# Kernel tuning notes

Hardware: AMD Instinct MI355X
Metric: run time of the kernel (lower is better)

Reference implementation:

```python
import jax, jax.numpy as jnp
import numpy as np

B, C = 20000, 8          # trees, children (leaves) per tree
WORD, TAG, MEM = 300, 50, 150


def gru_cell(x, h, w_ih, w_hh, b_ih, b_hh):
    # torch.nn.GRUCell math; gate order r, z, n
    gi = x @ w_ih.T + b_ih
    gh = h @ w_hh.T + b_hh
    ir, iz, i_n = jnp.split(gi, 3, axis=-1)
    hr, hz, hn = jnp.split(gh, 3, axis=-1)
    r = jax.nn.sigmoid(ir + hr)
    z = jax.nn.sigmoid(iz + hz)
    n = jnp.tanh(i_n + r * hn)
    return (1.0 - z) * n + z * h


def setup_inputs() -> dict:
    key = jax.random.key(0)
    ks = jax.random.split(key, 16)
    s = 0.05  # small init scale for weights
    return {
        "embs": jax.random.normal(ks[0], (B, C, WORD), jnp.float32),
        "tags": jax.random.normal(ks[1], (B, C, TAG), jnp.float32),
        "tag_parent": jax.random.normal(ks[2], (B, TAG), jnp.float32),
        "w_ih_leaf": jax.random.normal(ks[3], (3 * MEM, WORD + TAG), jnp.float32) * s,
        "w_hh_leaf": jax.random.normal(ks[4], (3 * MEM, MEM), jnp.float32) * s,
        "b_ih_leaf": jax.random.normal(ks[5], (3 * MEM,), jnp.float32) * s,
        "b_hh_leaf": jax.random.normal(ks[6], (3 * MEM,), jnp.float32) * s,
        "w_ih_child": jax.random.normal(ks[7], (3 * MEM, MEM + 2 * TAG), jnp.float32) * s,
        "w_hh_child": jax.random.normal(ks[8], (3 * MEM, MEM), jnp.float32) * s,
        "b_ih_child": jax.random.normal(ks[9], (3 * MEM,), jnp.float32) * s,
        "b_hh_child": jax.random.normal(ks[10], (3 * MEM,), jnp.float32) * s,
        "w_ih_node": jax.random.normal(ks[11], (3 * MEM, 1), jnp.float32) * s,
        "w_hh_node": jax.random.normal(ks[12], (3 * MEM, MEM), jnp.float32) * s,
        "b_ih_node": jax.random.normal(ks[13], (3 * MEM,), jnp.float32) * s,
        "b_hh_node": jax.random.normal(ks[14], (3 * MEM,), jnp.float32) * s,
    }


def reference(embs, tags, tag_parent,
              w_ih_leaf, w_hh_leaf, b_ih_leaf, b_hh_leaf,
              w_ih_child, w_hh_child, b_ih_child, b_hh_child,
              w_ih_node, w_hh_node, b_ih_node, b_hh_node):
    # 1) all leaves at once: GRUCell(concat(word, tag), h=0)  -> [B, C, MEM]
    x_leaf = jnp.concatenate([embs, tags], axis=-1)            # [B, C, WORD+TAG]
    h0 = jnp.zeros((B, C, MEM), x_leaf.dtype)
    leaf_h = gru_cell(x_leaf, h0, w_ih_leaf, w_hh_leaf, b_ih_leaf, b_hh_leaf)

    # 2) child inputs: concat(child state, child tag, parent tag)  -> [B, C, MEM+2*TAG]
    tp = jnp.broadcast_to(tag_parent[:, None, :], (B, C, TAG))
    x_child = jnp.concatenate([leaf_h, tags, tp], axis=-1)

    # 3) sequential left-to-right fold over children with children GRUCell
    def step(h, x_i):
        h_new = gru_cell(x_i, h, w_ih_child, w_hh_child, b_ih_child, b_hh_child)
        return h_new, None

    h_init = jnp.zeros((B, MEM), x_leaf.dtype)
    h_final, _ = jax.lax.scan(step, h_init, jnp.swapaxes(x_child, 0, 1))  # scan over C

    # 4) node GRUCell with x = zeros(1)
    x_zeros = jnp.zeros((B, 1), x_leaf.dtype)
    root = gru_cell(x_zeros, h_final, w_ih_node, w_hh_node, b_ih_node, b_hh_node)
    return root  # [B, MEM]
```

## Files before the change

### kernel.cpp

```cpp
#include <hip/hip_runtime.h>


typedef _Float16 f16;
typedef _Float16 f16x4 __attribute__((ext_vector_type(4)));
typedef _Float16 f16x8 __attribute__((ext_vector_type(8)));
typedef float f32x4 __attribute__((ext_vector_type(4)));

namespace {

constexpr int NTREE = 20000;
constexpr int CCH   = 8;
constexpr int WORD  = 300;
constexpr int TAGD  = 50;
constexpr int MEMD  = 150;
constexpr int NBLK  = 250;
constexpr int LBLK  = 313;

constexpr int KT_L = 11;
constexpr int KT_I = 8;
constexpr int KT_H = 5;
constexpr int KT_N = 5;
constexpr int NTILE = 30;

constexpr size_t OFF_WL   = 0;
constexpr size_t OFF_WI   = OFF_WL + (size_t)KT_L * NTILE * 64 * 16;
constexpr size_t OFF_WH   = OFF_WI + (size_t)KT_I * NTILE * 64 * 16;
constexpr size_t OFF_WN   = OFF_WH + (size_t)KT_H * NTILE * 64 * 16;
constexpr size_t OFF_BIAS = OFF_WN + (size_t)KT_N * NTILE * 64 * 16;
constexpr size_t OFF_DATA = OFF_BIAS + 16 * 160 * 4;

constexpr size_t TG_BYTES = 15360;
constexpr size_t C_STRIDE = (size_t)1250 * TG_BYTES;
constexpr size_t GI_BYTES = (size_t)CCH * C_STRIDE;
constexpr size_t WS_R3    = OFF_DATA + GI_BYTES;
constexpr int    HW_S  = 152;
constexpr size_t WS_R2 = OFF_DATA + (size_t)CCH * NTREE * HW_S * 2;


__device__ __forceinline__ float sigmoid_f(float x) {
  return 1.0f / (1.0f + __expf(-x));
}
__device__ __forceinline__ float tanh_f(float x) {
  float ax = fabsf(x);
  float e  = __expf(-2.0f * ax);
  float t  = (1.0f - e) / (1.0f + e);
  return copysignf(t, x);
}

__global__ void prep_kernel(const float* __restrict__ w_ih_leaf,
                            const float* __restrict__ b_ih_leaf,
                            const float* __restrict__ b_hh_leaf,
                            const float* __restrict__ w_ih_child,
                            const float* __restrict__ w_hh_child,
                            const float* __restrict__ b_ih_child,
                            const float* __restrict__ b_hh_child,
                            const float* __restrict__ w_hh_node,
                            const float* __restrict__ b_ih_node,
                            const float* __restrict__ b_hh_node,
                            char* __restrict__ ws) {
  const int NWL = KT_L * NTILE * 64;
  const int NWI = KT_I * NTILE * 64;
  const int NWH = KT_H * NTILE * 64;
  const int NWN = KT_N * NTILE * 64;
  int t = blockIdx.x * blockDim.x + threadIdx.x;

  if (t < NWL) {
    int kt = t / (NTILE * 64), rem = t % (NTILE * 64);
    int nt = rem / 64, l = rem % 64;
    int gate = nt / 10, jt = nt % 10;
    int j = jt * 16 + (l & 15);
    bool valid = j < MEMD;
    int g = gate * MEMD + (valid ? j : 0);
    f16x8 v;
#pragma unroll
    for (int e = 0; e < 8; ++e) {
      int k = kt * 32 + ((l >> 4) * 8) + e;
      v[e] = (f16)((valid && k < WORD + TAGD) ? w_ih_leaf[g * (WORD + TAGD) + k] : 0.0f);
    }
    ((f16x8*)(ws + OFF_WL))[t] = v;
    return;
  }
  t -= NWL;
  if (t < NWI) {
    int kt = t / (NTILE * 64), rem = t % (NTILE * 64);
    int nt = rem / 64, l = rem % 64;
    int gate = nt / 10, jt = nt % 10;
    int j = jt * 16 + (l & 15);
    bool valid = j < MEMD;
    int g = gate * MEMD + (valid ? j : 0);
    f16x8 v;
#pragma unroll
    for (int e = 0; e < 8; ++e) {
      int k = kt * 32 + ((l >> 4) * 8) + e;
      int src = (k < 150) ? k : (k >= 152 && k < 252) ? (k - 2) : -1;
      v[e] = (f16)((valid && src >= 0) ? w_ih_child[g * 250 + src] : 0.0f);
    }
    ((f16x8*)(ws + OFF_WI))[t] = v;
    return;
  }
  t -= NWI;
  if (t < NWH) {
    int kt = t / (NTILE * 64), rem = t % (NTILE * 64);
    int nt = rem / 64, l = rem % 64;
    int gate = nt / 10, jt = nt % 10;
    int j = jt * 16 + (l & 15);
    bool valid = j < MEMD;
    int g = gate * MEMD + (valid ? j : 0);
    f16x8 v;
#pragma unroll
    for (int e = 0; e < 8; ++e) {
      int k = kt * 32 + ((l >> 4) * 8) + e;
      v[e] = (f16)((valid && k < MEMD) ? w_hh_child[g * MEMD + k] : 0.0f);
    }
    ((f16x8*)(ws + OFF_WH))[t] = v;
    return;
  }
  t -= NWH;
  if (t < NWN) {
    int kt = t / (NTILE * 64), rem = t % (NTILE * 64);
    int nt = rem / 64, l = rem % 64;
    int gate = nt / 10, jt = nt % 10;
    int j = jt * 16 + (l & 15);
    bool valid = j < MEMD;
    int g = gate * MEMD + (valid ? j : 0);
    f16x8 v;
#pragma unroll
    for (int e = 0; e < 8; ++e) {
      int k = kt * 32 + ((l >> 4) * 8) + e;
      v[e] = (f16)((valid && k < MEMD) ? w_hh_node[g * MEMD + k] : 0.0f);
    }
    ((f16x8*)(ws + OFF_WN))[t] = v;
    return;
  }
  t -= NWN;
  if (t < 16 * 160) {
    int arr = t / 160, j = t % 160;
    float v = 0.0f;
    if (j < MEMD) {
      switch (arr) {
        case 0:  v = b_ih_leaf[j] + b_hh_leaf[j]; break;
        case 1:  v = b_ih_leaf[MEMD + j] + b_hh_leaf[MEMD + j]; break;
        case 2:  v = b_ih_leaf[2 * MEMD + j]; break;
        case 3:  v = b_hh_leaf[2 * MEMD + j]; break;
        case 4:  v = b_ih_child[j] + b_hh_child[j]; break;
        case 5:  v = b_ih_child[MEMD + j] + b_hh_child[MEMD + j]; break;
        case 6:  v = b_ih_child[2 * MEMD + j]; break;
        case 7:  v = b_hh_child[2 * MEMD + j]; break;
        case 8:  v = b_ih_node[j] + b_hh_node[j]; break;
        case 9:  v = b_ih_node[MEMD + j] + b_hh_node[MEMD + j]; break;
        case 10: v = b_ih_node[2 * MEMD + j]; break;
        case 11: v = b_hh_node[2 * MEMD + j]; break;
        case 12: v = b_ih_child[j]; break;
        case 13: v = b_ih_child[MEMD + j]; break;
        case 14: v = b_hh_child[j]; break;
        case 15: v = b_hh_child[MEMD + j]; break;
      }
    }
    ((float*)(ws + OFF_BIAS))[arr * 160 + j] = v;
  }
}

__global__ __launch_bounds__(640)
void leaf6_kernel(const float* __restrict__ embs,
                  const float* __restrict__ tags,
                  const float* __restrict__ tag_parent,
                  char* __restrict__ ws) {
  __shared__ f16 buf[64 * 360];
  f16* xle = buf;
  f16* xch = buf;

  const f16x8* WL   = (const f16x8*)(ws + OFF_WL);
  const f16x8* WI   = (const f16x8*)(ws + OFF_WI);
  const float* BIAS = (const float*)(ws + OFF_BIAS);

  const int tid = threadIdx.x, lane = tid & 63, w = tid >> 6;
  const int blk = blockIdx.x, c = blockIdx.y, t0 = blk * 64;
  const int arow = lane & 15, acol8 = (lane >> 4) * 8, qrow = (lane >> 4) * 4;
  const int j = w * 16 + arow;
  const bool jok = j < MEMD;

  for (int i = tid; i < 64 * 75; i += 640) {
    int r = i / 75, k4 = i - r * 75;
    int row = min(t0 + r, NTREE - 1);
    float4 v = *(const float4*)(embs + ((size_t)row * CCH + c) * WORD + 4 * k4);
    f16* p = xle + r * 360 + 4 * k4;
    p[0] = (f16)v.x; p[1] = (f16)v.y; p[2] = (f16)v.z; p[3] = (f16)v.w;
  }
  for (int i = tid; i < 64 * 25; i += 640) {
    int r = i / 25, k2 = i - r * 25;
    int row = min(t0 + r, NTREE - 1);
    float2 v = *(const float2*)(tags + ((size_t)row * CCH + c) * TAGD + 2 * k2);
    xle[r * 360 + 300 + 2 * k2]     = (f16)v.x;
    xle[r * 360 + 300 + 2 * k2 + 1] = (f16)v.y;
  }
  if (tid < 64) {
    xle[tid * 360 + 350] = (f16)0.0f;
    xle[tid * 360 + 351] = (f16)0.0f;
  }
  __syncthreads();

  f32x4 acc[3][4];
#pragma unroll
  for (int g = 0; g < 3; ++g)
#pragma unroll
    for (int m = 0; m < 4; ++m) acc[g][m] = 0.f;

  for (int kt = 0; kt < KT_L; ++kt) {
    f16x8 a0 = *(const f16x8*)(xle + kt * 32 + acol8 + (arow)      * 360);
    f16x8 a1 = *(const f16x8*)(xle + kt * 32 + acol8 + (16 + arow) * 360);
    f16x8 a2 = *(const f16x8*)(xle + kt * 32 + acol8 + (32 + arow) * 360);
    f16x8 a3 = *(const f16x8*)(xle + kt * 32 + acol8 + (48 + arow) * 360);
#pragma unroll
    for (int g = 0; g < 3; ++g) {
      f16x8 b = WL[(kt * NTILE + g * 10 + w) * 64 + lane];
      acc[g][0] = __builtin_amdgcn_mfma_f32_16x16x32_f16(a0, b, acc[g][0], 0, 0, 0);
      acc[g][1] = __builtin_amdgcn_mfma_f32_16x16x32_f16(a1, b, acc[g][1], 0, 0, 0);
      acc[g][2] = __builtin_amdgcn_mfma_f32_16x16x32_f16(a2, b, acc[g][2], 0, 0, 0);
      acc[g][3] = __builtin_amdgcn_mfma_f32_16x16x32_f16(a3, b, acc[g][3], 0, 0, 0);
    }
  }
  __syncthreads();

  {
    const float bLr = BIAS[j], bLz = BIAS[160 + j];
    const float bLi = BIAS[320 + j], bLh = BIAS[480 + j];
#pragma unroll
    for (int m = 0; m < 4; ++m)
#pragma unroll
      for (int q = 0; q < 4; ++q) {
        int row = 16 * m + qrow + q;
        float rg = sigmoid_f(acc[0][m][q] + bLr);
        float zg = sigmoid_f(acc[1][m][q] + bLz);
        float ng = tanh_f(acc[2][m][q] + bLi + rg * bLh);
        if (jok) xch[row * 264 + j] = (f16)((1.0f - zg) * ng);
      }
  }
  for (int i = tid; i < 64 * 25; i += 640) {
    int r = i / 25, k2 = i - r * 25;
    int row = min(t0 + r, NTREE - 1);
    float2 v = *(const float2*)(tags + ((size_t)row * CCH + c) * TAGD + 2 * k2);
    xch[r * 264 + 152 + 2 * k2] = (f16)v.x;
    xch[r * 264 + 153 + 2 * k2] = (f16)v.y;
  }
  for (int i = tid; i < 64 * 25; i += 640) {
    int r = i / 25, k2 = i - r * 25;
    int row = min(t0 + r, NTREE - 1);
    float2 v = *(const float2*)(tag_parent + (size_t)row * TAGD + 2 * k2);
    xch[r * 264 + 202 + 2 * k2] = (f16)v.x;
    xch[r * 264 + 203 + 2 * k2] = (f16)v.y;
  }
  for (int i = tid; i < 64 * 6; i += 640) {
    int r = i / 6, k = i - r * 6;
    int col = (k < 2) ? (150 + k) : (250 + k);
    xch[r * 264 + col] = (f16)0.0f;
  }
  __syncthreads();

#pragma unroll
  for (int g = 0; g < 3; ++g)
#pragma unroll
    for (int m = 0; m < 4; ++m) acc[g][m] = 0.f;

  for (int kt = 0; kt < KT_I; ++kt) {
    f16x8 a0 = *(const f16x8*)(xch + kt * 32 + acol8 + (arow)      * 264);
    f16x8 a1 = *(const f16x8*)(xch + kt * 32 + acol8 + (16 + arow) * 264);
    f16x8 a2 = *(const f16x8*)(xch + kt * 32 + acol8 + (32 + arow) * 264);
    f16x8 a3 = *(const f16x8*)(xch + kt * 32 + acol8 + (48 + arow) * 264);
#pragma unroll
    for (int g = 0; g < 3; ++g) {
      f16x8 b = WI[(kt * NTILE + g * 10 + w) * 64 + lane];
      acc[g][0] = __builtin_amdgcn_mfma_f32_16x16x32_f16(a0, b, acc[g][0], 0, 0, 0);
      acc[g][1] = __builtin_amdgcn_mfma_f32_16x16x32_f16(a1, b, acc[g][1], 0, 0, 0);
      acc[g][2] = __builtin_amdgcn_mfma_f32_16x16x32_f16(a2, b, acc[g][2], 0, 0, 0);
      acc[g][3] = __builtin_amdgcn_mfma_f32_16x16x32_f16(a3, b, acc[g][3], 0, 0, 0);
    }
  }

  {
    const float bi[3] = {BIAS[12 * 160 + j], BIAS[13 * 160 + j], BIAS[6 * 160 + j]};
#pragma unroll
    for (int m = 0; m < 4; ++m) {
      if (t0 + 16 * m < NTREE) {
        int tg = blk * 4 + m;
        char* base = ws + OFF_DATA + (size_t)c * C_STRIDE + (size_t)tg * TG_BYTES +
                     (size_t)lane * 8;
#pragma unroll
        for (int g = 0; g < 3; ++g) {
          f16x4 v;
#pragma unroll
          for (int q = 0; q < 4; ++q) v[q] = (f16)(acc[g][m][q] + bi[g]);
          *(f16x4*)(base + (size_t)(g * 10 + w) * 512) = v;
        }
      }
    }
  }
}

__global__ __launch_bounds__(640, 1)
void fold6_kernel(const char* __restrict__ ws,
                  float* __restrict__ out) {
  __shared__ f16 hls[80 * 168];

  const f16x8* WH   = (const f16x8*)(ws + OFF_WH);
  const f16x8* WN   = (const f16x8*)(ws + OFF_WN);
  const float* BIAS = (const float*)(ws + OFF_BIAS);

  const int tid = threadIdx.x, lane = tid & 63, w = tid >> 6;
  const int blk = blockIdx.x, t0 = blk * 80;
  const int arow = lane & 15, acol8 = (lane >> 4) * 8, qrow = (lane >> 4) * 4;
  const int j = w * 16 + arow;
  const bool jok = j < MEMD;

  const float bhr = BIAS[14 * 160 + j], bhz = BIAS[15 * 160 + j], bhn = BIAS[7 * 160 + j];
  const float bNr = BIAS[8 * 160 + j],  bNz = BIAS[9 * 160 + j];
  const float bNi = BIAS[10 * 160 + j], bNh = BIAS[11 * 160 + j];

  for (int i = tid; i < 80 * 18; i += 640) {
    int r = i / 18;
    hls[r * 168 + 150 + (i - r * 18)] = (f16)0.0f;
  }

  f16x8 whr[5], whz[5], whn[5];
#pragma unroll
  for (int kt = 0; kt < KT_H; ++kt) {
    whr[kt] = WH[(kt * NTILE + w) * 64 + lane];
    whz[kt] = WH[(kt * NTILE + 10 + w) * 64 + lane];
    whn[kt] = WH[(kt * NTILE + 20 + w) * 64 + lane];
  }

  const char* gbase = ws + OFF_DATA + (size_t)(blk * 5) * TG_BYTES +
                      (size_t)w * 512 + (size_t)lane * 8;

  f32x4 hp[5];
#pragma unroll
  for (int m = 0; m < 5; ++m) hp[m] = 0.f;

#pragma unroll
  for (int c = 0; c < CCH; ++c) {
    f16x4 gbuf[15];
#pragma unroll
    for (int m = 0; m < 5; ++m)
#pragma unroll
      for (int g = 0; g < 3; ++g)
        gbuf[m * 3 + g] = *(const f16x4*)(gbase + (size_t)c * C_STRIDE +
                                          (size_t)m * TG_BYTES + (size_t)g * 5120);

    f32x4 aR[5], aZ[5], aNh[5];
#pragma unroll
    for (int m = 0; m < 5; ++m) { aR[m] = 0.f; aZ[m] = 0.f; aNh[m] = 0.f; }

    if (c != 0) {
#pragma unroll
      for (int kt = 0; kt < KT_H; ++kt) {
        const f16* ab = hls + kt * 32 + acol8;
#pragma unroll
        for (int m = 0; m < 5; ++m) {
          f16x8 a = *(const f16x8*)(ab + (16 * m + arow) * 168);
          aR[m]  = __builtin_amdgcn_mfma_f32_16x16x32_f16(a, whr[kt], aR[m], 0, 0, 0);
          aZ[m]  = __builtin_amdgcn_mfma_f32_16x16x32_f16(a, whz[kt], aZ[m], 0, 0, 0);
          aNh[m] = __builtin_amdgcn_mfma_f32_16x16x32_f16(a, whn[kt], aNh[m], 0, 0, 0);
        }
      }
      __syncthreads();
    }

#pragma unroll
    for (int m = 0; m < 5; ++m)
#pragma unroll
      for (int q = 0; q < 4; ++q) {
        int row = 16 * m + qrow + q;
        float rg = sigmoid_f((float)gbuf[m * 3 + 0][q] + aR[m][q] + bhr);
        float zg = sigmoid_f((float)gbuf[m * 3 + 1][q] + aZ[m][q] + bhz);
        float ng = tanh_f((float)gbuf[m * 3 + 2][q] + rg * (aNh[m][q] + bhn));
        float h  = (1.0f - zg) * ng + zg * hp[m][q];
        hp[m][q] = h;
        if (jok) hls[row * 168 + j] = (f16)h;
      }
    __syncthreads();
  }

  f32x4 aR[5], aZ[5], aNh[5];
#pragma unroll
  for (int m = 0; m < 5; ++m) { aR[m] = 0.f; aZ[m] = 0.f; aNh[m] = 0.f; }
  for (int kt = 0; kt < KT_N; ++kt) {
    f16x8 br = WN[(kt * NTILE + w) * 64 + lane];
    f16x8 bz = WN[(kt * NTILE + 10 + w) * 64 + lane];
    f16x8 bn = WN[(kt * NTILE + 20 + w) * 64 + lane];
    const f16* ab = hls + kt * 32 + acol8;
#pragma unroll
    for (int m = 0; m < 5; ++m) {
      f16x8 a = *(const f16x8*)(ab + (16 * m + arow) * 168);
      aR[m]  = __builtin_amdgcn_mfma_f32_16x16x32_f16(a, br, aR[m], 0, 0, 0);
      aZ[m]  = __builtin_amdgcn_mfma_f32_16x16x32_f16(a, bz, aZ[m], 0, 0, 0);
      aNh[m] = __builtin_amdgcn_mfma_f32_16x16x32_f16(a, bn, aNh[m], 0, 0, 0);
    }
  }
#pragma unroll
  for (int m = 0; m < 5; ++m)
#pragma unroll
    for (int q = 0; q < 4; ++q) {
      int row = 16 * m + qrow + q;
      float rg = sigmoid_f(aR[m][q] + bNr);
      float zg = sigmoid_f(aZ[m][q] + bNz);
      float ng = tanh_f(bNi + rg * (aNh[m][q] + bNh));
      float o  = (1.0f - zg) * ng + zg * hp[m][q];
      if (jok) out[(size_t)(t0 + row) * MEMD + j] = o;
    }
}

namespace r2 {

__global__ __launch_bounds__(640)
void leaf_kernel(const float* __restrict__ embs,
                 const float* __restrict__ tags,
                 char* __restrict__ ws) {
  __shared__ f16 xle[80 * 360];
  const f16x8* WL   = (const f16x8*)(ws + OFF_WL);
  const float* BIAS = (const float*)(ws + OFF_BIAS);
  f16* hws = (f16*)(ws + OFF_DATA);

  const int tid = threadIdx.x, lane = tid & 63, w = tid >> 6;
  const int c = blockIdx.y, t0 = blockIdx.x * 80;
  const int arow = lane & 15, acol8 = (lane >> 4) * 8, qrow = (lane >> 4) * 4;
  const int j = w * 16 + (lane & 15);

  for (int i = tid; i < 80 * 150; i += 640) {
    int r = i / 150, k2 = i - r * 150;
    float2 v = *(const float2*)(embs + ((size_t)(t0 + r) * CCH + c) * WORD + 2 * k2);
    xle[r * 360 + 2 * k2]     = (f16)v.x;
    xle[r * 360 + 2 * k2 + 1] = (f16)v.y;
  }
  for (int i = tid; i < 80 * 25; i += 640) {
    int r = i / 25, k2 = i - r * 25;
    float2 v = *(const float2*)(tags + ((size_t)(t0 + r) * CCH + c) * TAGD + 2 * k2);
    xle[r * 360 + 300 + 2 * k2]     = (f16)v.x;
    xle[r * 360 + 300 + 2 * k2 + 1] = (f16)v.y;
  }
  for (int i = tid; i < 80; i += 640) {
    xle[i * 360 + 350] = (f16)0.0f;
    xle[i * 360 + 351] = (f16)0.0f;
  }
  __syncthreads();

  f32x4 aR[5], aZ[5], aN[5];
#pragma unroll
  for (int m = 0; m < 5; ++m) { aR[m] = 0.f; aZ[m] = 0.f; aN[m] = 0.f; }
  for (int kt = 0; kt < KT_L; ++kt) {
    f16x8 br = WL[(kt * NTILE + w) * 64 + lane];
    f16x8 bz = WL[(kt * NTILE + 10 + w) * 64 + lane];
    f16x8 bn = WL[(kt * NTILE + 20 + w) * 64 + lane];
    const f16* ab = xle + kt * 32 + acol8;
#pragma unroll
    for (int m = 0; m < 5; ++m) {
      f16x8 a = *(const f16x8*)(ab + (16 * m + arow) * 360);
      aR[m] = __builtin_amdgcn_mfma_f32_16x16x32_f16(a, br, aR[m], 0, 0, 0);
      aZ[m] = __builtin_amdgcn_mfma_f32_16x16x32_f16(a, bz, aZ[m], 0, 0, 0);
      aN[m] = __builtin_amdgcn_mfma_f32_16x16x32_f16(a, bn, aN[m], 0, 0, 0);
    }
  }
  const float bLr = BIAS[j], bLz = BIAS[160 + j], bLi = BIAS[320 + j], bLh = BIAS[480 + j];
#pragma unroll
  for (int m = 0; m < 5; ++m) {
#pragma unroll
    for (int q = 0; q < 4; ++q) {
      int row = 16 * m + qrow + q;
      float rg = sigmoid_f(aR[m][q] + bLr);
      float zg = sigmoid_f(aZ[m][q] + bLz);
      float ng = tanh_f(aN[m][q] + bLi + rg * bLh);
      float h  = (1.0f - zg) * ng;
      if (j < HW_S)
        hws[((size_t)c * NTREE + t0 + row) * HW_S + j] = (f16)(j < MEMD ? h : 0.0f);
    }
  }
}

__global__ __launch_bounds__(640)
void fold_kernel(const float* __restrict__ tags,
                 const float* __restrict__ tag_parent,
                 const char* __restrict__ ws,
                 float* __restrict__ out) {
  extern __shared__ char fsm[];
  f16* xch0 = (f16*)fsm;
  f16* xch1 = xch0 + 80 * 264;
  f16* hls  = xch1 + 80 * 264;

  const f16x8* WI   = (const f16x8*)(ws + OFF_WI);
  const f16x8* WH   = (const f16x8*)(ws + OFF_WH);
  const f16x8* WN   = (const f16x8*)(ws + OFF_WN);
  const float* BIAS = (const float*)(ws + OFF_BIAS);
  const f16*   hws  = (const f16*)(ws + OFF_DATA);

  const int tid = threadIdx.x, lane = tid & 63, w = tid >> 6;
  const int t0 = blockIdx.x * 80;
  const int arow = lane & 15, acol8 = (lane >> 4) * 8, qrow = (lane >> 4) * 4;
  const int j = w * 16 + (lane & 15);
  const bool jok = j < MEMD;

  const float bCr = BIAS[4 * 160 + j], bCz = BIAS[5 * 160 + j];
  const float bCi = BIAS[6 * 160 + j], bCh = BIAS[7 * 160 + j];
  const float bNr = BIAS[8 * 160 + j], bNz = BIAS[9 * 160 + j];
  const float bNi = BIAS[10 * 160 + j], bNh = BIAS[11 * 160 + j];

  for (int i = tid; i < 1680; i += 640) ((int4*)hls)[i] = make_int4(0, 0, 0, 0);
  for (int i = tid; i < 80 * 25; i += 640) {
    int r = i / 25, k2 = i - r * 25;
    float2 v = *(const float2*)(tag_parent + (size_t)(t0 + r) * TAGD + 2 * k2);
    f16 a = (f16)v.x, b = (f16)v.y;
    xch0[r * 264 + 202 + 2 * k2] = a; xch0[r * 264 + 203 + 2 * k2] = b;
    xch1[r * 264 + 202 + 2 * k2] = a; xch1[r * 264 + 203 + 2 * k2] = b;
  }
  for (int i = tid; i < 80 * 4; i += 640) {
    int r = i >> 2, k = i & 3;
    xch0[r * 264 + 252 + k] = (f16)0.0f;
    xch1[r * 264 + 252 + k] = (f16)0.0f;
  }
#pragma unroll
  for (int s = 0; s < 3; ++s) {
    int i = tid + 640 * s;
    if (i < 1520) {
      int r = i / 19, q = i - r * 19;
      *(f16x8*)(xch0 + r * 264 + 8 * q) =
          *(const f16x8*)(hws + ((size_t)(t0 + r)) * HW_S + 8 * q);
    }
  }
#pragma unroll
  for (int s = 0; s < 4; ++s) {
    int i = tid + 640 * s;
    if (i < 2000) {
      int r = i / 25, k2 = i - r * 25;
      float2 v = *(const float2*)(tags + ((size_t)(t0 + r) * CCH) * TAGD + 2 * k2);
      xch0[r * 264 + 152 + 2 * k2] = (f16)v.x;
      xch0[r * 264 + 153 + 2 * k2] = (f16)v.y;
    }
  }
  __syncthreads();

  f32x4 hp[5];
#pragma unroll
  for (int m = 0; m < 5; ++m) hp[m] = 0.f;

  f16* xc = xch0;
  f16* xa = xch1;

  for (int c = 0; c < CCH; ++c) {
    f16x8 ph[3];
    float2 pt[4];
    if (c < 7) {
#pragma unroll
      for (int s = 0; s < 3; ++s) {
        int i = tid + 640 * s;
        if (i < 1520) {
          int r = i / 19, q = i - r * 19;
          ph[s] = *(const f16x8*)(hws + ((size_t)(c + 1) * NTREE + t0 + r) * HW_S + 8 * q);
        }
      }
#pragma unroll
      for (int s = 0; s < 4; ++s) {
        int i = tid + 640 * s;
        if (i < 2000) {
          int r = i / 25, k2 = i - r * 25;
          pt[s] = *(const float2*)(tags + ((size_t)(t0 + r) * CCH + (c + 1)) * TAGD + 2 * k2);
        }
      }
    }

    f32x4 aR[5], aZ[5], aNi[5], aNh[5];
#pragma unroll
    for (int m = 0; m < 5; ++m) { aR[m] = 0.f; aZ[m] = 0.f; aNi[m] = 0.f; aNh[m] = 0.f; }
    for (int kt = 0; kt < KT_I; ++kt) {
      f16x8 br = WI[(kt * NTILE + w) * 64 + lane];
      f16x8 bz = WI[(kt * NTILE + 10 + w) * 64 + lane];
      f16x8 bn = WI[(kt * NTILE + 20 + w) * 64 + lane];
      const f16* ab = xc + kt * 32 + acol8;
#pragma unroll
      for (int m = 0; m < 5; ++m) {
        f16x8 a = *(const f16x8*)(ab + (16 * m + arow) * 264);
        aR[m]  = __builtin_amdgcn_mfma_f32_16x16x32_f16(a, br, aR[m], 0, 0, 0);
        aZ[m]  = __builtin_amdgcn_mfma_f32_16x16x32_f16(a, bz, aZ[m], 0, 0, 0);
        aNi[m] = __builtin_amdgcn_mfma_f32_16x16x32_f16(a, bn, aNi[m], 0, 0, 0);
      }
    }
    for (int kt = 0; kt < KT_H; ++kt) {
      f16x8 br = WH[(kt * NTILE + w) * 64 + lane];
      f16x8 bz = WH[(kt * NTILE + 10 + w) * 64 + lane];
      f16x8 bn = WH[(kt * NTILE + 20 + w) * 64 + lane];
      const f16* ab = hls + kt * 32 + acol8;
#pragma unroll
      for (int m = 0; m < 5; ++m) {
        f16x8 a = *(const f16x8*)(ab + (16 * m + arow) * 168);
        aR[m]  = __builtin_amdgcn_mfma_f32_16x16x32_f16(a, br, aR[m], 0, 0, 0);
        aZ[m]  = __builtin_amdgcn_mfma_f32_16x16x32_f16(a, bz, aZ[m], 0, 0, 0);
        aNh[m] = __builtin_amdgcn_mfma_f32_16x16x32_f16(a, bn, aNh[m], 0, 0, 0);
      }
    }
    __syncthreads();

    if (c < 7) {
#pragma unroll
      for (int s = 0; s < 3; ++s) {
        int i = tid + 640 * s;
        if (i < 1520) {
          int r = i / 19, q = i - r * 19;
          *(f16x8*)(xa + r * 264 + 8 * q) = ph[s];
        }
      }
#pragma unroll
      for (int s = 0; s < 4; ++s) {
        int i = tid + 640 * s;
        if (i < 2000) {
          int r = i / 25, k2 = i - r * 25;
          xa[r * 264 + 152 + 2 * k2] = (f16)pt[s].x;
          xa[r * 264 + 153 + 2 * k2] = (f16)pt[s].y;
        }
      }
    }

#pragma unroll
    for (int m = 0; m < 5; ++m) {
#pragma unroll
      for (int q = 0; q < 4; ++q) {
        int row = 16 * m + qrow + q;
        float rg = sigmoid_f(aR[m][q] + bCr);
        float zg = sigmoid_f(aZ[m][q] + bCz);
        float ng = tanh_f(aNi[m][q] + bCi + rg * (aNh[m][q] + bCh));
        float h  = (1.0f - zg) * ng + zg * hp[m][q];
        hp[m][q] = h;
        if (jok) hls[row * 168 + j] = (f16)h;
      }
    }
    __syncthreads();
    f16* tsw = xc; xc = xa; xa = tsw;
  }

  f32x4 aR[5], aZ[5], aNh[5];
#pragma unroll
  for (int m = 0; m < 5; ++m) { aR[m] = 0.f; aZ[m] = 0.f; aNh[m] = 0.f; }
  for (int kt = 0; kt < KT_N; ++kt) {
    f16x8 br = WN[(kt * NTILE + w) * 64 + lane];
    f16x8 bz = WN[(kt * NTILE + 10 + w) * 64 + lane];
    f16x8 bn = WN[(kt * NTILE + 20 + w) * 64 + lane];
    const f16* ab = hls + kt * 32 + acol8;
#pragma unroll
    for (int m = 0; m < 5; ++m) {
      f16x8 a = *(const f16x8*)(ab + (16 * m + arow) * 168);
      aR[m]  = __builtin_amdgcn_mfma_f32_16x16x32_f16(a, br, aR[m], 0, 0, 0);
      aZ[m]  = __builtin_amdgcn_mfma_f32_16x16x32_f16(a, bz, aZ[m], 0, 0, 0);
      aNh[m] = __builtin_amdgcn_mfma_f32_16x16x32_f16(a, bn, aNh[m], 0, 0, 0);
    }
  }
#pragma unroll
  for (int m = 0; m < 5; ++m) {
#pragma unroll
    for (int q = 0; q < 4; ++q) {
      int row = 16 * m + qrow + q;
      float rg = sigmoid_f(aR[m][q] + bNr);
      float zg = sigmoid_f(aZ[m][q] + bNz);
      float ng = tanh_f(bNi + rg * (aNh[m][q] + bNh));
      float o  = (1.0f - zg) * ng + zg * hp[m][q];
      if (jok) out[(size_t)(t0 + row) * MEMD + j] = o;
    }
  }
}

}

}

extern "C" void kernel_launch(void* const* d_in, const int* in_sizes, int n_in,
                              void* d_out, int out_size, void* d_ws, size_t ws_size,
                              hipStream_t stream) {
  const float* embs       = (const float*)d_in[0];
  const float* tags       = (const float*)d_in[1];
  const float* tag_parent = (const float*)d_in[2];
  const float* w_ih_leaf  = (const float*)d_in[3];
  const float* b_ih_leaf  = (const float*)d_in[5];
  const float* b_hh_leaf  = (const float*)d_in[6];
  const float* w_ih_child = (const float*)d_in[7];
  const float* w_hh_child = (const float*)d_in[8];
  const float* b_ih_child = (const float*)d_in[9];
  const float* b_hh_child = (const float*)d_in[10];
  const float* w_hh_node  = (const float*)d_in[12];
  const float* b_ih_node  = (const float*)d_in[13];
  const float* b_hh_node  = (const float*)d_in[14];
  float* out = (float*)d_out;
  char*  ws  = (char*)d_ws;

  prep_kernel<<<228, 256, 0, stream>>>(w_ih_leaf, b_ih_leaf, b_hh_leaf,
                                       w_ih_child, w_hh_child, b_ih_child, b_hh_child,
                                       w_hh_node, b_ih_node, b_hh_node, ws);

  if (ws_size >= WS_R3) {
    leaf6_kernel<<<dim3(LBLK, CCH), 640, 0, stream>>>(embs, tags, tag_parent, ws);
    fold6_kernel<<<NBLK, 640, 0, stream>>>(ws, out);
  } else {
    r2::leaf_kernel<<<dim3(250, CCH), 640, 0, stream>>>(embs, tags, ws);
    constexpr int FOLD_LDS = (2 * 80 * 264 + 80 * 168) * 2;
    hipFuncSetAttribute((const void*)r2::fold_kernel,
                        hipFuncAttributeMaxDynamicSharedMemorySize, FOLD_LDS);
    r2::fold_kernel<<<250, 640, FOLD_LDS, stream>>>(tags, tag_parent, ws, out);
  }
}
```

Measured before the change: 391.1 us.

## Process two children per leaf block with register prefetch; double-buffer fold hidden state

The leaf kernel now handles two children per block. The second child's embeddings and tags are prefetched into registers while the first child's GEMMs run, and tag_parent is loaded once and reused for both children. The fold kernel ping-pongs the hidden state between two LDS buffers, which removes one barrier per step. In exchange the leaf grid is halved to about 1252 blocks of 640 threads, with more LDS and register pressure per block (launch_bounds 640,1), which may reduce how well latency is hidden.

```diff
diff --git a/kernel.cpp b/kernel.cpp
--- a/kernel.cpp
+++ b/kernel.cpp
@@ -160,56 +160,93 @@
   }
 }
 
-__global__ __launch_bounds__(640)
-void leaf6_kernel(const float* __restrict__ embs,
-                  const float* __restrict__ tags,
-                  const float* __restrict__ tag_parent,
-                  char* __restrict__ ws) {
-  __shared__ f16 buf[64 * 360];
-  f16* xle = buf;
-  f16* xch = buf;
+__global__ __launch_bounds__(640, 1)
+void leaf11_kernel(const float* __restrict__ embs,
+                   const float* __restrict__ tags,
+                   const float* __restrict__ tag_parent,
+                   char* __restrict__ ws) {
+  __shared__ f16 bufA[64 * 360];
+  __shared__ f16 bufB[64 * 360];
 
   const f16x8* WL   = (const f16x8*)(ws + OFF_WL);
   const f16x8* WI   = (const f16x8*)(ws + OFF_WI);
   const float* BIAS = (const float*)(ws + OFF_BIAS);
 
   const int tid = threadIdx.x, lane = tid & 63, w = tid >> 6;
-  const int blk = blockIdx.x, c = blockIdx.y, t0 = blk * 64;
+  const int blk = blockIdx.x, t0 = blk * 64;
+  const int c0 = blockIdx.y * 2, c1 = c0 + 1;
   const int arow = lane & 15, acol8 = (lane >> 4) * 8, qrow = (lane >> 4) * 4;
   const int j = w * 16 + arow;
   const bool jok = j < MEMD;
 
+  const float bLr = BIAS[j], bLz = BIAS[160 + j];
+  const float bLi = BIAS[320 + j], bLh = BIAS[480 + j];
+  const float biC[3] = {BIAS[12 * 160 + j], BIAS[13 * 160 + j], BIAS[6 * 160 + j]};
+
+  float2 tp[3];
+#pragma unroll
+  for (int s = 0; s < 3; ++s) {
+    int i = tid + 640 * s;
+    tp[s] = make_float2(0.0f, 0.0f);
+    if (i < 1600) {
+      int r = i / 25, k2 = i - (i / 25) * 25;
+      int row = min(t0 + r, NTREE - 1);
+      tp[s] = *(const float2*)(tag_parent + (size_t)row * TAGD + 2 * k2);
+    }
+  }
+
   for (int i = tid; i < 64 * 75; i += 640) {
     int r = i / 75, k4 = i - r * 75;
     int row = min(t0 + r, NTREE - 1);
-    float4 v = *(const float4*)(embs + ((size_t)row * CCH + c) * WORD + 4 * k4);
-    f16* p = xle + r * 360 + 4 * k4;
+    float4 v = *(const float4*)(embs + ((size_t)row * CCH + c0) * WORD + 4 * k4);
+    f16* p = bufA + r * 360 + 4 * k4;
     p[0] = (f16)v.x; p[1] = (f16)v.y; p[2] = (f16)v.z; p[3] = (f16)v.w;
   }
   for (int i = tid; i < 64 * 25; i += 640) {
     int r = i / 25, k2 = i - r * 25;
     int row = min(t0 + r, NTREE - 1);
-    float2 v = *(const float2*)(tags + ((size_t)row * CCH + c) * TAGD + 2 * k2);
-    xle[r * 360 + 300 + 2 * k2]     = (f16)v.x;
-    xle[r * 360 + 300 + 2 * k2 + 1] = (f16)v.y;
+    float2 v = *(const float2*)(tags + ((size_t)row * CCH + c0) * TAGD + 2 * k2);
+    bufA[r * 360 + 300 + 2 * k2]     = (f16)v.x;
+    bufA[r * 360 + 300 + 2 * k2 + 1] = (f16)v.y;
   }
   if (tid < 64) {
-    xle[tid * 360 + 350] = (f16)0.0f;
-    xle[tid * 360 + 351] = (f16)0.0f;
+    bufA[tid * 360 + 350] = (f16)0.0f;
+    bufA[tid * 360 + 351] = (f16)0.0f;
   }
   __syncthreads();
 
+  float4 pe[8];
+  float2 pt[3];
+#pragma unroll
+  for (int s = 0; s < 8; ++s) {
+    int i = tid + 640 * s;
+    if (i < 4800) {
+      int r = i / 75, k4 = i - r * 75;
+      int row = min(t0 + r, NTREE - 1);
+      pe[s] = *(const float4*)(embs + ((size_t)row * CCH + c1) * WORD + 4 * k4);
+    }
+  }
+#pragma unroll
+  for (int s = 0; s < 3; ++s) {
+    int i = tid + 640 * s;
+    if (i < 1600) {
+      int r = i / 25, k2 = i - (i / 25) * 25;
+      int row = min(t0 + r, NTREE - 1);
+      pt[s] = *(const float2*)(tags + ((size_t)row * CCH + c1) * TAGD + 2 * k2);
+    }
+  }
+
   f32x4 acc[3][4];
+
 #pragma unroll
   for (int g = 0; g < 3; ++g)
 #pragma unroll
     for (int m = 0; m < 4; ++m) acc[g][m] = 0.f;
-
   for (int kt = 0; kt < KT_L; ++kt) {
-    f16x8 a0 = *(const f16x8*)(xle + kt * 32 + acol8 + (arow)      * 360);
-    f16x8 a1 = *(const f16x8*)(xle + kt * 32 + acol8 + (16 + arow) * 360);
-    f16x8 a2 = *(const f16x8*)(xle + kt * 32 + acol8 + (32 + arow) * 360);
-    f16x8 a3 = *(const f16x8*)(xle + kt * 32 + acol8 + (48 + arow) * 360);
+    f16x8 a0 = *(const f16x8*)(bufA + kt * 32 + acol8 + (arow)      * 360);
+    f16x8 a1 = *(const f16x8*)(bufA + kt * 32 + acol8 + (16 + arow) * 360);
+    f16x8 a2 = *(const f16x8*)(bufA + kt * 32 + acol8 + (32 + arow) * 360);
+    f16x8 a3 = *(const f16x8*)(bufA + kt * 32 + acol8 + (48 + arow) * 360);
 #pragma unroll
     for (int g = 0; g < 3; ++g) {
       f16x8 b = WL[(kt * NTILE + g * 10 + w) * 64 + lane];
@@ -221,38 +258,58 @@
   }
   __syncthreads();
 
-  {
-    const float bLr = BIAS[j], bLz = BIAS[160 + j];
-    const float bLi = BIAS[320 + j], bLh = BIAS[480 + j];
-#pragma unroll
-    for (int m = 0; m < 4; ++m)
-#pragma unroll
-      for (int q = 0; q < 4; ++q) {
-        int row = 16 * m + qrow + q;
-        float rg = sigmoid_f(acc[0][m][q] + bLr);
-        float zg = sigmoid_f(acc[1][m][q] + bLz);
-        float ng = tanh_f(acc[2][m][q] + bLi + rg * bLh);
-        if (jok) xch[row * 264 + j] = (f16)((1.0f - zg) * ng);
-      }
-  }
+#pragma unroll
+  for (int s = 0; s < 8; ++s) {
+    int i = tid + 640 * s;
+    if (i < 4800) {
+      int r = i / 75, k4 = i - (i / 75) * 75;
+      f16* p = bufB + r * 360 + 4 * k4;
+      p[0] = (f16)pe[s].x; p[1] = (f16)pe[s].y; p[2] = (f16)pe[s].z; p[3] = (f16)pe[s].w;
+    }
+  }
+#pragma unroll
+  for (int s = 0; s < 3; ++s) {
+    int i = tid + 640 * s;
+    if (i < 1600) {
+      int r = i / 25, k2 = i - (i / 25) * 25;
+      bufB[r * 360 + 300 + 2 * k2]     = (f16)pt[s].x;
+      bufB[r * 360 + 300 + 2 * k2 + 1] = (f16)pt[s].y;
+    }
+  }
+  if (tid < 64) {
+    bufB[tid * 360 + 350] = (f16)0.0f;
+    bufB[tid * 360 + 351] = (f16)0.0f;
+  }
+#pragma unroll
+  for (int m = 0; m < 4; ++m)
+#pragma unroll
+    for (int q = 0; q < 4; ++q) {
+      int row = 16 * m + qrow + q;
+      float rg = sigmoid_f(acc[0][m][q] + bLr);
+      float zg = sigmoid_f(acc[1][m][q] + bLz);
+      float ng = tanh_f(acc[2][m][q] + bLi + rg * bLh);
+      if (jok) bufA[row * 264 + j] = (f16)((1.0f - zg) * ng);
+    }
   for (int i = tid; i < 64 * 25; i += 640) {
     int r = i / 25, k2 = i - r * 25;
     int row = min(t0 + r, NTREE - 1);
-    float2 v = *(const float2*)(tags + ((size_t)row * CCH + c) * TAGD + 2 * k2);
-    xch[r * 264 + 152 + 2 * k2] = (f16)v.x;
-    xch[r * 264 + 153 + 2 * k2] = (f16)v.y;
-  }
-  for (int i = tid; i < 64 * 25; i += 640) {
-    int r = i / 25, k2 = i - r * 25;
-    int row = min(t0 + r, NTREE - 1);
-    float2 v = *(const float2*)(tag_parent + (size_t)row * TAGD + 2 * k2);
-    xch[r * 264 + 202 + 2 * k2] = (f16)v.x;
-    xch[r * 264 + 203 + 2 * k2] = (f16)v.y;
+    float2 v = *(const float2*)(tags + ((size_t)row * CCH + c0) * TAGD + 2 * k2);
+    bufA[r * 264 + 152 + 2 * k2] = (f16)v.x;
+    bufA[r * 264 + 153 + 2 * k2] = (f16)v.y;
+  }
+#pragma unroll
+  for (int s = 0; s < 3; ++s) {
+    int i = tid + 640 * s;
+    if (i < 1600) {
+      int r = i / 25, k2 = i - (i / 25) * 25;
+      bufA[r * 264 + 202 + 2 * k2] = (f16)tp[s].x;
+      bufA[r * 264 + 203 + 2 * k2] = (f16)tp[s].y;
+    }
   }
   for (int i = tid; i < 64 * 6; i += 640) {
     int r = i / 6, k = i - r * 6;
     int col = (k < 2) ? (150 + k) : (250 + k);
-    xch[r * 264 + col] = (f16)0.0f;
+    bufA[r * 264 + col] = (f16)0.0f;
   }
   __syncthreads();
 
@@ -260,12 +317,11 @@
   for (int g = 0; g < 3; ++g)
 #pragma unroll
     for (int m = 0; m < 4; ++m) acc[g][m] = 0.f;
-
   for (int kt = 0; kt < KT_I; ++kt) {
-    f16x8 a0 = *(const f16x8*)(xch + kt * 32 + acol8 + (arow)      * 264);
-    f16x8 a1 = *(const f16x8*)(xch + kt * 32 + acol8 + (16 + arow) * 264);
-    f16x8 a2 = *(const f16x8*)(xch + kt * 32 + acol8 + (32 + arow) * 264);
-    f16x8 a3 = *(const f16x8*)(xch + kt * 32 + acol8 + (48 + arow) * 264);
+    f16x8 a0 = *(const f16x8*)(bufA + kt * 32 + acol8 + (arow)      * 264);
+    f16x8 a1 = *(const f16x8*)(bufA + kt * 32 + acol8 + (16 + arow) * 264);
+    f16x8 a2 = *(const f16x8*)(bufA + kt * 32 + acol8 + (32 + arow) * 264);
+    f16x8 a3 = *(const f16x8*)(bufA + kt * 32 + acol8 + (48 + arow) * 264);
 #pragma unroll
     for (int g = 0; g < 3; ++g) {
       f16x8 b = WI[(kt * NTILE + g * 10 + w) * 64 + lane];
@@ -275,31 +331,109 @@
       acc[g][3] = __builtin_amdgcn_mfma_f32_16x16x32_f16(a3, b, acc[g][3], 0, 0, 0);
     }
   }
-
-  {
-    const float bi[3] = {BIAS[12 * 160 + j], BIAS[13 * 160 + j], BIAS[6 * 160 + j]};
-#pragma unroll
-    for (int m = 0; m < 4; ++m) {
-      if (t0 + 16 * m < NTREE) {
-        int tg = blk * 4 + m;
-        char* base = ws + OFF_DATA + (size_t)c * C_STRIDE + (size_t)tg * TG_BYTES +
-                     (size_t)lane * 8;
-#pragma unroll
-        for (int g = 0; g < 3; ++g) {
-          f16x4 v;
-#pragma unroll
-          for (int q = 0; q < 4; ++q) v[q] = (f16)(acc[g][m][q] + bi[g]);
-          *(f16x4*)(base + (size_t)(g * 10 + w) * 512) = v;
-        }
+#pragma unroll
+  for (int m = 0; m < 4; ++m) {
+    if (t0 + 16 * m < NTREE) {
+      int tg = blk * 4 + m;
+      char* base = ws + OFF_DATA + (size_t)c0 * C_STRIDE + (size_t)tg * TG_BYTES +
+                   (size_t)lane * 8;
+#pragma unroll
+      for (int g = 0; g < 3; ++g) {
+        f16x4 v;
+#pragma unroll
+        for (int q = 0; q < 4; ++q) v[q] = (f16)(acc[g][m][q] + biC[g]);
+        *(f16x4*)(base + (size_t)(g * 10 + w) * 512) = v;
+      }
+    }
+  }
+
+#pragma unroll
+  for (int g = 0; g < 3; ++g)
+#pragma unroll
+    for (int m = 0; m < 4; ++m) acc[g][m] = 0.f;
+  for (int kt = 0; kt < KT_L; ++kt) {
+    f16x8 a0 = *(const f16x8*)(bufB + kt * 32 + acol8 + (arow)      * 360);
+    f16x8 a1 = *(const f16x8*)(bufB + kt * 32 + acol8 + (16 + arow) * 360);
+    f16x8 a2 = *(const f16x8*)(bufB + kt * 32 + acol8 + (32 + arow) * 360);
+    f16x8 a3 = *(const f16x8*)(bufB + kt * 32 + acol8 + (48 + arow) * 360);
+#pragma unroll
+    for (int g = 0; g < 3; ++g) {
+      f16x8 b = WL[(kt * NTILE + g * 10 + w) * 64 + lane];
+      acc[g][0] = __builtin_amdgcn_mfma_f32_16x16x32_f16(a0, b, acc[g][0], 0, 0, 0);
+      acc[g][1] = __builtin_amdgcn_mfma_f32_16x16x32_f16(a1, b, acc[g][1], 0, 0, 0);
+      acc[g][2] = __builtin_amdgcn_mfma_f32_16x16x32_f16(a2, b, acc[g][2], 0, 0, 0);
+      acc[g][3] = __builtin_amdgcn_mfma_f32_16x16x32_f16(a3, b, acc[g][3], 0, 0, 0);
+    }
+  }
+  __syncthreads();
+
+#pragma unroll
+  for (int m = 0; m < 4; ++m)
+#pragma unroll
+    for (int q = 0; q < 4; ++q) {
+      int row = 16 * m + qrow + q;
+      float rg = sigmoid_f(acc[0][m][q] + bLr);
+      float zg = sigmoid_f(acc[1][m][q] + bLz);
+      float ng = tanh_f(acc[2][m][q] + bLi + rg * bLh);
+      if (jok) bufB[row * 264 + j] = (f16)((1.0f - zg) * ng);
+    }
+#pragma unroll
+  for (int s = 0; s < 3; ++s) {
+    int i = tid + 640 * s;
+    if (i < 1600) {
+      int r = i / 25, k2 = i - (i / 25) * 25;
+      bufB[r * 264 + 152 + 2 * k2] = (f16)pt[s].x;
+      bufB[r * 264 + 153 + 2 * k2] = (f16)pt[s].y;
+      bufB[r * 264 + 202 + 2 * k2] = (f16)tp[s].x;
+      bufB[r * 264 + 203 + 2 * k2] = (f16)tp[s].y;
+    }
+  }
+  for (int i = tid; i < 64 * 6; i += 640) {
+    int r = i / 6, k = i - r * 6;
+    int col = (k < 2) ? (150 + k) : (250 + k);
+    bufB[r * 264 + col] = (f16)0.0f;
+  }
+  __syncthreads();
+
+#pragma unroll
+  for (int g = 0; g < 3; ++g)
+#pragma unroll
+    for (int m = 0; m < 4; ++m) acc[g][m] = 0.f;
+  for (int kt = 0; kt < KT_I; ++kt) {
+    f16x8 a0 = *(const f16x8*)(bufB + kt * 32 + acol8 + (arow)      * 264);
+    f16x8 a1 = *(const f16x8*)(bufB + kt * 32 + acol8 + (16 + arow) * 264);
+    f16x8 a2 = *(const f16x8*)(bufB + kt * 32 + acol8 + (32 + arow) * 264);
+    f16x8 a3 = *(const f16x8*)(bufB + kt * 32 + acol8 + (48 + arow) * 264);
+#pragma unroll
+    for (int g = 0; g < 3; ++g) {
+      f16x8 b = WI[(kt * NTILE + g * 10 + w) * 64 + lane];
+      acc[g][0] = __builtin_amdgcn_mfma_f32_16x16x32_f16(a0, b, acc[g][0], 0, 0, 0);
+      acc[g][1] = __builtin_amdgcn_mfma_f32_16x16x32_f16(a1, b, acc[g][1], 0, 0, 0);
+      acc[g][2] = __builtin_amdgcn_mfma_f32_16x16x32_f16(a2, b, acc[g][2], 0, 0, 0);
+      acc[g][3] = __builtin_amdgcn_mfma_f32_16x16x32_f16(a3, b, acc[g][3], 0, 0, 0);
+    }
+  }
+#pragma unroll
+  for (int m = 0; m < 4; ++m) {
+    if (t0 + 16 * m < NTREE) {
+      int tg = blk * 4 + m;
+      char* base = ws + OFF_DATA + (size_t)c1 * C_STRIDE + (size_t)tg * TG_BYTES +
+                   (size_t)lane * 8;
+#pragma unroll
+      for (int g = 0; g < 3; ++g) {
+        f16x4 v;
+#pragma unroll
+        for (int q = 0; q < 4; ++q) v[q] = (f16)(acc[g][m][q] + biC[g]);
+        *(f16x4*)(base + (size_t)(g * 10 + w) * 512) = v;
       }
     }
   }
 }
 
 __global__ __launch_bounds__(640, 1)
-void fold6_kernel(const char* __restrict__ ws,
-                  float* __restrict__ out) {
-  __shared__ f16 hls[80 * 168];
+void fold11_kernel(const char* __restrict__ ws,
+                   float* __restrict__ out) {
+  __shared__ f16 hls[2 * 80 * 168];
 
   const f16x8* WH   = (const f16x8*)(ws + OFF_WH);
   const f16x8* WN   = (const f16x8*)(ws + OFF_WN);
@@ -315,9 +449,10 @@
   const float bNr = BIAS[8 * 160 + j],  bNz = BIAS[9 * 160 + j];
   const float bNi = BIAS[10 * 160 + j], bNh = BIAS[11 * 160 + j];
 
-  for (int i = tid; i < 80 * 18; i += 640) {
-    int r = i / 18;
-    hls[r * 168 + 150 + (i - r * 18)] = (f16)0.0f;
+  for (int i = tid; i < 2 * 80 * 18; i += 640) {
+    int b = i / (80 * 18), rem = i - b * (80 * 18);
+    int r = rem / 18;
+    hls[b * 80 * 168 + r * 168 + 150 + (rem - r * 18)] = (f16)0.0f;
   }
 
   f16x8 whr[5], whz[5], whn[5];
@@ -345,6 +480,9 @@
         gbuf[m * 3 + g] = *(const f16x4*)(gbase + (size_t)c * C_STRIDE +
                                           (size_t)m * TG_BYTES + (size_t)g * 5120);
 
+    const f16* hcur = hls + (c & 1) * 80 * 168;
+    f16*       hnxt = hls + ((c + 1) & 1) * 80 * 168;
+
     f32x4 aR[5], aZ[5], aNh[5];
 #pragma unroll
     for (int m = 0; m < 5; ++m) { aR[m] = 0.f; aZ[m] = 0.f; aNh[m] = 0.f; }
@@ -352,7 +490,7 @@
     if (c != 0) {
 #pragma unroll
       for (int kt = 0; kt < KT_H; ++kt) {
-        const f16* ab = hls + kt * 32 + acol8;
+        const f16* ab = hcur + kt * 32 + acol8;
 #pragma unroll
         for (int m = 0; m < 5; ++m) {
           f16x8 a = *(const f16x8*)(ab + (16 * m + arow) * 168);
@@ -361,7 +499,6 @@
           aNh[m] = __builtin_amdgcn_mfma_f32_16x16x32_f16(a, whn[kt], aNh[m], 0, 0, 0);
         }
       }
-      __syncthreads();
     }
 
 #pragma unroll
@@ -374,11 +511,12 @@
         float ng = tanh_f((float)gbuf[m * 3 + 2][q] + rg * (aNh[m][q] + bhn));
         float h  = (1.0f - zg) * ng + zg * hp[m][q];
         hp[m][q] = h;
-        if (jok) hls[row * 168 + j] = (f16)h;
+        if (jok) hnxt[row * 168 + j] = (f16)h;
       }
     __syncthreads();
   }
 
+  const f16* hfin = hls;
   f32x4 aR[5], aZ[5], aNh[5];
 #pragma unroll
   for (int m = 0; m < 5; ++m) { aR[m] = 0.f; aZ[m] = 0.f; aNh[m] = 0.f; }
@@ -386,7 +524,7 @@
     f16x8 br = WN[(kt * NTILE + w) * 64 + lane];
     f16x8 bz = WN[(kt * NTILE + 10 + w) * 64 + lane];
     f16x8 bn = WN[(kt * NTILE + 20 + w) * 64 + lane];
-    const f16* ab = hls + kt * 32 + acol8;
+    const f16* ab = hfin + kt * 32 + acol8;
 #pragma unroll
     for (int m = 0; m < 5; ++m) {
       f16x8 a = *(const f16x8*)(ab + (16 * m + arow) * 168);
@@ -690,8 +828,8 @@
                                        w_hh_node, b_ih_node, b_hh_node, ws);
 
   if (ws_size >= WS_R3) {
-    leaf6_kernel<<<dim3(LBLK, CCH), 640, 0, stream>>>(embs, tags, tag_parent, ws);
-    fold6_kernel<<<NBLK, 640, 0, stream>>>(ws, out);
+    leaf11_kernel<<<dim3(LBLK, CCH / 2), 640, 0, stream>>>(embs, tags, tag_parent, ws);
+    fold11_kernel<<<NBLK, 640, 0, stream>>>(ws, out);
   } else {
     r2::leaf_kernel<<<dim3(250, CCH), 640, 0, stream>>>(embs, tags, ws);
     constexpr int FOLD_LDS = (2 * 80 * 264 + 80 * 168) * 2;
```

After: 470.6 us. 1.2x slower.
